# Kernel tuning notes

Measured on AMD Instinct MI355X. Metric: run time of the kernel, lower is better.

## Reference

```python
import jax, jax.numpy as jnp
import numpy as np

NUM_ENTITIES = 40000
NUM_RELATIONS = 500
NUM_EDGES = 400000
ENT_DIM = 50
REL_DIM = 50
NUM_HEADS = 8
UNITS = [150, 300]
NEG_SLOPE = 0.2


def setup_inputs() -> dict:
    key = jax.random.key(0)
    ks = jax.random.split(key, 12)
    h_index = jax.random.randint(ks[0], (NUM_EDGES,), 0, NUM_ENTITIES)
    r_index = jax.random.randint(ks[1], (NUM_EDGES,), 0, NUM_RELATIONS)
    t_index = jax.random.randint(ks[2], (NUM_EDGES,), 0, NUM_ENTITIES)
    std_e = np.sqrt(1.0 / ENT_DIM).astype(np.float32)
    std_r = np.sqrt(1.0 / REL_DIM).astype(np.float32)
    entity_embeddings = jax.random.truncated_normal(ks[3], -2.0, 2.0, (NUM_ENTITIES, ENT_DIM), jnp.float32) * std_e
    relation_embeddings = jax.random.truncated_normal(ks[4], -2.0, 2.0, (NUM_RELATIONS, REL_DIM), jnp.float32) * std_r
    # gat0: input ent dim 50, rel dim 50 -> concat 150, units 150
    c0 = ENT_DIM + REL_DIM + ENT_DIM
    gat0_kernel = jax.random.normal(ks[5], (NUM_HEADS, c0, UNITS[0]), jnp.float32) * (1.0 / np.sqrt(c0))
    gat0_attn = jax.random.normal(ks[6], (NUM_HEADS, UNITS[0]), jnp.float32) * (1.0 / np.sqrt(UNITS[0]))
    gat0_rel_kernel = jax.random.normal(ks[7], (REL_DIM, UNITS[0]), jnp.float32) * (1.0 / np.sqrt(REL_DIM))
    # gat1: input ent dim 8*150=1200, rel dim 150 -> concat 2550, units 300
    e1 = NUM_HEADS * UNITS[0]
    c1 = e1 + UNITS[0] + e1
    gat1_kernel = jax.random.normal(ks[8], (NUM_HEADS, c1, UNITS[1]), jnp.float32) * (1.0 / np.sqrt(c1))
    gat1_attn = jax.random.normal(ks[9], (NUM_HEADS, UNITS[1]), jnp.float32) * (1.0 / np.sqrt(UNITS[1]))
    gat1_rel_kernel = jax.random.normal(ks[10], (UNITS[0], UNITS[1]), jnp.float32) * (1.0 / np.sqrt(UNITS[0]))
    dense_w = jax.random.normal(ks[11], (ENT_DIM, UNITS[1]), jnp.float32) * (1.0 / np.sqrt(ENT_DIM))
    dense_b = jnp.zeros((UNITS[1],), jnp.float32)
    return dict(h_index=h_index, r_index=r_index, t_index=t_index,
                entity_embeddings=entity_embeddings, relation_embeddings=relation_embeddings,
                gat0_kernel=gat0_kernel, gat0_attn=gat0_attn, gat0_rel_kernel=gat0_rel_kernel,
                gat1_kernel=gat1_kernel, gat1_attn=gat1_attn, gat1_rel_kernel=gat1_rel_kernel,
                dense_w=dense_w, dense_b=dense_b)


def _kbgat_layer(h, r, t, ent, rel, kernel, attn, rel_kernel):
    """One KBGAT layer. kernel: [H, De+Dr+De, U] acting on concat(ent[h], rel[r], ent[t]).
    Split kernel so projections happen at node/relation level (equivalent, avoids E x concat_dim)."""
    N = ent.shape[0]
    De = ent.shape[1]
    Dr = rel.shape[1]
    outs = []
    for hd in range(kernel.shape[0]):
        W = kernel[hd]
        Wh, Wr, Wt = W[:De], W[De:De + Dr], W[De + Dr:]
        # message c_{hrt} = W [ent_h ; rel_r ; ent_t] : [E, U]
        c = (ent @ Wh)[h] + (rel @ Wr)[r] + (ent @ Wt)[t]
        s = jax.nn.leaky_relu(c @ attn[hd], NEG_SLOPE)  # [E]
        # segment softmax over triples sharing the same head entity
        m = jax.ops.segment_max(s, h, num_segments=N)
        e = jnp.exp(s - m[h])
        d = jax.ops.segment_sum(e, h, num_segments=N)
        a = e / (d[h] + 1e-10)
        agg = jax.ops.segment_sum(a[:, None] * c, h, num_segments=N)  # [N, U]
        outs.append(jax.nn.elu(agg))
    rel_out = rel @ rel_kernel
    return outs, rel_out


def reference(h_index, r_index, t_index, entity_embeddings, relation_embeddings,
              gat0_kernel, gat0_attn, gat0_rel_kernel,
              gat1_kernel, gat1_attn, gat1_rel_kernel, dense_w, dense_b):
    h = h_index.astype(jnp.int32)
    r = r_index.astype(jnp.int32)
    t = t_index.astype(jnp.int32)
    # dropout rate is 0.0 / inference -> identity
    outs0, rel0 = _kbgat_layer(h, r, t, entity_embeddings, relation_embeddings,
                               gat0_kernel, gat0_attn, gat0_rel_kernel)
    feat = jnp.concatenate(outs0, axis=-1)  # [N, H*U0]
    outs1, rel1 = _kbgat_layer(h, r, t, feat, rel0, gat1_kernel, gat1_attn, gat1_rel_kernel)
    ent_out = outs1[0]
    for o in outs1[1:]:
        ent_out = ent_out + o  # add_n over heads
    ent_out = ent_out + (entity_embeddings @ dense_w + dense_b)  # dense residual
    return ent_out, rel1
```

## Files before the change

kernel.cpp:

```cpp
#include <hip/hip_runtime.h>
#include <hip/hip_bf16.h>
#include <math.h>
#include <stdint.h>

typedef __attribute__((ext_vector_type(8))) __bf16 bf16x8;
typedef __attribute__((ext_vector_type(4))) float f32x4;
typedef unsigned short us;

#define GLP(p) ((__attribute__((address_space(1))) void*)(p))
#define LDP(p) ((__attribute__((address_space(3))) void*)(p))

static __device__ __forceinline__ float b2f(us u) {
    return __uint_as_float(((unsigned int)u) << 16);
}
static __device__ __forceinline__ us f2b(float f) {
    unsigned int x = __float_as_uint(f);
    return (us)((x + 0x7fffu + ((x >> 16) & 1u)) >> 16);
}

__global__ __launch_bounds__(256) void sentinel(float* out, int n, float v) {
    int i = blockIdx.x * 256 + threadIdx.x;
    if (i < n) out[i] = v;
}

__global__ __launch_bounds__(256) void zero_featpad(us* __restrict__ feat) {
    int idx = blockIdx.x * 256 + threadIdx.x;
    if (idx < 40064 * 16) {
        int n = idx >> 4, c = idx & 15;
        feat[(size_t)n * 1216 + 1200 + c] = 0;
    }
}
__global__ __launch_bounds__(256) void zero_x0pad(us* __restrict__ X0) {
    int idx = blockIdx.x * 256 + threadIdx.x;
    if (idx < 4 * 64 * 192) {
        int w = idx / (64 * 192);
        int rem = idx % (64 * 192);
        int rr = rem / 192, c = rem % 192;
        X0[((size_t)w * 40064 + 40000 + rr) * 192 + c] = 0;
    }
}

__global__ __launch_bounds__(256) void count_edges(const int* __restrict__ h, int* __restrict__ counts) {
    int e = blockIdx.x * 256 + threadIdx.x;
    if (e < 400000) atomicAdd(&counts[h[e]], 1);
}

__global__ void scan40k(const int* __restrict__ counts, int* __restrict__ rs) {
    __shared__ int part[1024];
    int tid = threadIdx.x;
    int base = tid * 40;
    int s = 0;
    for (int i = 0; i < 40; ++i) { int idx = base + i; s += (idx < 40000) ? counts[idx] : 0; }
    part[tid] = s;
    __syncthreads();
    for (int off = 1; off < 1024; off <<= 1) {
        int v = (tid >= off) ? part[tid - off] : 0;
        __syncthreads();
        part[tid] += v;
        __syncthreads();
    }
    int run = (tid == 0) ? 0 : part[tid - 1];
    for (int i = 0; i < 40; ++i) {
        int idx = base + i;
        if (idx < 40000) { rs[idx] = run; run += counts[idx]; }
    }
    if (tid == 1023) rs[40000] = part[1023];
}

__global__ __launch_bounds__(256) void scatter_edges(const int* __restrict__ h, const int* __restrict__ rs,
                                                     int* __restrict__ cursor, int* __restrict__ se) {
    int e = blockIdx.x * 256 + threadIdx.x;
    if (e < 400000) {
        int n = h[e];
        int pos = rs[n] + atomicAdd(&cursor[n], 1);
        se[pos] = e;
    }
}

__global__ __launch_bounds__(256) void pack_ent(const float* __restrict__ ent, us* __restrict__ A0) {
    int idx = blockIdx.x * 256 + threadIdx.x;
    if (idx >= 40064 * 64) return;
    int n = idx >> 6, k = idx & 63;
    A0[idx] = (n < 40000 && k < 50) ? f2b(ent[n * 50 + k]) : (us)0;
}

__global__ __launch_bounds__(256) void build_V0(const float* __restrict__ g0k, const float* __restrict__ attn0,
                                                float* __restrict__ V0) {
    int idx = blockIdx.x * 256 + threadIdx.x;
    if (idx >= 50 * 24) return;
    int k = idx / 24, g = idx % 24;
    int part = g >> 3, hd = g & 7;
    int row = k + (part == 1 ? 100 : (part == 2 ? 50 : 0));
    float s = 0.f;
    for (int u = 0; u < 150; ++u)
        s += g0k[(hd * 150 + row) * 150 + u] * attn0[hd * 150 + u];
    V0[idx] = s;
}

__global__ __launch_bounds__(256) void build_VT0(const float* __restrict__ g0k, const float* __restrict__ attn0,
                                                 us* __restrict__ VT0) {
    int idx = blockIdx.x * 256 + threadIdx.x;
    if (idx >= 128 * 64) return;
    int g = idx >> 6, k = idx & 63;
    us v = 0;
    if (g < 16 && k < 50) {
        int part = g >> 3, hd = g & 7;
        int row = part ? (100 + k) : k;
        float s = 0.f;
        for (int u = 0; u < 150; ++u)
            s += g0k[(hd * 150 + row) * 150 + u] * attn0[hd * 150 + u];
        v = f2b(s);
    }
    VT0[idx] = v;
}

__global__ __launch_bounds__(256) void build_VT1(const float* __restrict__ g1k, const float* __restrict__ attn1,
                                                 us* __restrict__ VT1) {
    int idx = blockIdx.x * 256 + threadIdx.x;
    if (idx >= 128 * 1216) return;
    int g = idx / 1216, k = idx % 1216;
    us v = 0;
    if (g < 16 && k < 1200) {
        int part = g >> 3, hd = g & 7;
        int row = part ? (1350 + k) : k;
        float s = 0.f;
        for (int u = 0; u < 300; ++u)
            s += g1k[((size_t)hd * 2550 + row) * 300 + u] * attn1[hd * 300 + u];
        v = f2b(s);
    }
    VT1[idx] = v;
}

__global__ __launch_bounds__(256) void build_Vr1(const float* __restrict__ g1k, const float* __restrict__ attn1,
                                                 float* __restrict__ Vr1) {
    int idx = blockIdx.x * 256 + threadIdx.x;
    if (idx >= 150 * 8) return;
    int k = idx / 8, hd = idx % 8;
    float s = 0.f;
    for (int u = 0; u < 300; ++u)
        s += g1k[((size_t)hd * 2550 + 1200 + k) * 300 + u] * attn1[hd * 300 + u];
    Vr1[idx] = s;
}

__global__ __launch_bounds__(256) void scalar_proj(const void* __restrict__ Av, int aIsF32, int lda, int K,
                                                   const float* __restrict__ V, int ldv, int col0, int G,
                                                   float* __restrict__ out) {
    __shared__ float arow[1216];
    long n = blockIdx.x;
    if (aIsF32) {
        const float* A = (const float*)Av;
        for (int k = threadIdx.x; k < K; k += 256) arow[k] = A[n * lda + k];
    } else {
        const us* A = (const us*)Av;
        for (int k = threadIdx.x; k < K; k += 256) arow[k] = b2f(A[n * lda + k]);
    }
    __syncthreads();
    int g = threadIdx.x >> 4;
    int sl = threadIdx.x & 15;
    if (g < G) {
        float s = 0.f;
        for (int k = sl; k < K; k += 16) s += arow[k] * V[k * ldv + col0 + g];
        for (int off = 8; off; off >>= 1) s += __shfl_down(s, off, 16);
        if (sl == 0) out[n * G + g] = s;
    }
}

__global__ __launch_bounds__(256) void edge_stats(const int* __restrict__ rs, const int* __restrict__ se,
                                                  const int* __restrict__ rIdx, const int* __restrict__ tIdx,
                                                  const float* __restrict__ sc, const float* __restrict__ arr,
                                                  us* __restrict__ eAT, float* __restrict__ sfac) {
    int tid = blockIdx.x * 256 + threadIdx.x;
    if (tid >= 40000 * 8) return;
    int n = tid >> 3, hd = tid & 7;
    float ah = sc[n * 16 + hd];
    int p0 = rs[n], p1 = rs[n + 1];
    float m = -INFINITY, d = 0.f;
    for (int p = p0; p < p1; ++p) {
        int e = se[p];
        float s = ah + arr[rIdx[e] * 8 + hd] + sc[tIdx[e] * 16 + 8 + hd];
        s = (s > 0.f) ? s : 0.2f * s;
        if (s > m) { d = d * expf(m - s) + 1.f; m = s; }
        else d += expf(s - m);
    }
    float inv = 1.f / (d + 1e-10f);
    us* ea = eAT + (size_t)hd * 400000;
    for (int p = p0; p < p1; ++p) {
        int e = se[p];
        float s = ah + arr[rIdx[e] * 8 + hd] + sc[tIdx[e] * 16 + 8 + hd];
        s = (s > 0.f) ? s : 0.2f * s;
        ea[p] = f2b(expf(s - m) * inv);
    }
    sfac[tid] = d * inv;
}

__global__ __launch_bounds__(256) void agg0x4(int g, const int* __restrict__ rs, const int* __restrict__ se,
                                              const int* __restrict__ rIdx, const int* __restrict__ tIdx,
                                              const us* __restrict__ eAT, const float* __restrict__ sfac,
                                              const float* __restrict__ ent, const float* __restrict__ rel,
                                              us* __restrict__ X0) {
    __shared__ int sr[128], st[128];
    __shared__ float sa[4][128];
    long n = blockIdx.x;
    int tid = threadIdx.x;
    int lane = tid & 63, wave = tid >> 6;
    int hd = 4 * g + wave;
    int k = lane;
    float ev = (k < 50) ? ent[n * 50 + k] : 0.f;
    float xh = sfac[n * 8 + hd] * ev;
    float ra = 0.f, ta = 0.f;
    int p0 = rs[n], p1 = rs[n + 1];
    for (int c0 = p0; c0 < p1; c0 += 128) {
        int cnt = min(128, p1 - c0);
        __syncthreads();
        if (tid < cnt) {
            int e = se[c0 + tid];
            sr[tid] = rIdx[e];
            st[tid] = tIdx[e];
#pragma unroll
            for (int w = 0; w < 4; ++w)
                sa[w][tid] = b2f(eAT[(size_t)(4 * g + w) * 400000 + c0 + tid]);
        }
        __syncthreads();
#pragma unroll 2
        for (int i = 0; i < cnt; ++i) {
            float a = sa[wave][i];
            int r = sr[i], t = st[i];
            if (k < 50) {
                ra += a * rel[r * 50 + k];
                ta += a * ent[(long)t * 50 + k];
            }
        }
    }
    us* row = X0 + ((size_t)wave * 40064 + n) * 192;
    if (k < 50) { row[k] = f2b(xh); row[50 + k] = f2b(ra); row[100 + k] = f2b(ta); }
    if (lane < 42) row[150 + lane] = 0;
}

__global__ __launch_bounds__(256) void build_B0T8(const float* __restrict__ g0k, us* __restrict__ B) {
    int idx = blockIdx.x * 256 + threadIdx.x;
    if (idx >= 8 * 256 * 192) return;
    int hd = idx / (256 * 192);
    int u = (idx / 192) % 256, k = idx % 192;
    us v = 0;
    if (u < 150 && k < 150) v = f2b(g0k[((size_t)hd * 150 + k) * 150 + u]);
    B[idx] = v;
}

__global__ __launch_bounds__(256) void build_B1Th2(int g, const float* __restrict__ g1k, us* __restrict__ B) {
    int idx = blockIdx.x * 256 + threadIdx.x;
    if (idx >= 1280 * 1216) return;
    int j = idx / 1216, k = idx % 1216;
    us v = 0;
    if (j < 1216 && k < 1200) {
        int blk = j / 304, u = j % 304;
        if (u < 300) {
            int hd = 2 * g + (blk & 1);
            int row = (blk >= 2) ? (1350 + k) : k;
            v = f2b(g1k[((size_t)hd * 2550 + row) * 300 + u]);
        }
    }
    B[idx] = v;
}

#define GEMM_BODY(EPILOG)                                                                       \
    __shared__ __align__(16) us As[2][128 * 64];                                                \
    __shared__ __align__(16) us Bs[2][128 * 64];                                                \
    const int tid = threadIdx.x;                                                                \
    const int lane = tid & 63, wave = tid >> 6;                                                 \
    const int wr = wave >> 1, wc = wave & 1;                                                    \
    const int r16 = lane & 15, g4 = lane >> 4;                                                  \
    const long bm = blockIdx.y, bn = blockIdx.x;                                                \
    f32x4 acc[4][4];                                                                            \
    _Pragma("unroll") for (int m = 0; m < 4; ++m)                                               \
        _Pragma("unroll") for (int n = 0; n < 4; ++n) acc[m][n] = (f32x4){0.f, 0.f, 0.f, 0.f};  \
    auto stage = [&](int buf, int kt) {                                                         \
        _Pragma("unroll") for (int i = 0; i < 4; ++i) {                                         \
            int idx = tid + i * 256;                                                            \
            int row = idx >> 3, sub = idx & 7;                                                  \
            int scol = ((sub ^ (row & 7)) << 3);                                                \
            const us* ga = A + (bm * 128 + row) * (long)K + kt + scol;                          \
            __builtin_amdgcn_global_load_lds(GLP(ga), LDP(&As[buf][idx * 8]), 16, 0, 0);        \
        }                                                                                       \
        _Pragma("unroll") for (int i = 0; i < 4; ++i) {                                         \
            int idx = tid + i * 256;                                                            \
            int row = idx >> 3, sub = idx & 7;                                                  \
            int scol = ((sub ^ (row & 7)) << 3);                                                \
            const us* gb = BT + (bn * 128 + row) * (long)K + kt + scol;                         \
            __builtin_amdgcn_global_load_lds(GLP(gb), LDP(&Bs[buf][idx * 8]), 16, 0, 0);        \
        }                                                                                       \
    };                                                                                          \
    const int nt = K >> 6;                                                                      \
    stage(0, 0);                                                                                \
    const int sxor = (r16 & 7) << 3;                                                            \
    for (int t = 0; t < nt; ++t) {                                                              \
        int cur = t & 1;                                                                        \
        if (t + 1 < nt) {                                                                       \
            stage(cur ^ 1, (t + 1) << 6);                                                       \
            asm volatile("s_waitcnt vmcnt(8)" ::: "memory");                                    \
        } else {                                                                                \
            asm volatile("s_waitcnt vmcnt(0)" ::: "memory");                                    \
        }                                                                                       \
        __builtin_amdgcn_s_barrier();                                                           \
        asm volatile("" ::: "memory");                                                          \
        _Pragma("unroll") for (int kk = 0; kk < 2; ++kk) {                                      \
            bf16x8 af[4], bfr[4];                                                               \
            _Pragma("unroll") for (int m = 0; m < 4; ++m)                                       \
                af[m] = *(const bf16x8*)&As[cur][(wr * 64 + m * 16 + r16) * 64 +                \
                                               ((kk * 32 + g4 * 8) ^ sxor)];                    \
            _Pragma("unroll") for (int n = 0; n < 4; ++n)                                       \
                bfr[n] = *(const bf16x8*)&Bs[cur][(wc * 64 + n * 16 + r16) * 64 +               \
                                                ((kk * 32 + g4 * 8) ^ sxor)];                   \
            _Pragma("unroll") for (int m = 0; m < 4; ++m)                                       \
                _Pragma("unroll") for (int n = 0; n < 4; ++n)                                   \
                    acc[m][n] = __builtin_amdgcn_mfma_f32_16x16x32_bf16(af[m], bfr[n],          \
                                                                        acc[m][n], 0, 0, 0);    \
        }                                                                                       \
        asm volatile("" ::: "memory");                                                          \
        __builtin_amdgcn_s_barrier();                                                           \
    }                                                                                           \
    _Pragma("unroll") for (int m = 0; m < 4; ++m)                                               \
        _Pragma("unroll") for (int n = 0; n < 4; ++n)                                           \
            _Pragma("unroll") for (int j = 0; j < 4; ++j) { EPILOG }

__global__ __launch_bounds__(256) void gemm_bt(const us* __restrict__ A_, const us* __restrict__ BT_,
                                               us* __restrict__ C, int K, int ldc, int nColReal,
                                               int colOff0, int colOffZ, long aStrideZ, long btStrideZ,
                                               int act) {
    const int z = blockIdx.z;
    const us* A = A_ + (size_t)z * aStrideZ;
    const us* BT = BT_ + (size_t)z * btStrideZ;
    const int colBase = colOff0 + z * colOffZ;
    GEMM_BODY(
        int cc = (int)bn * 128 + wc * 64 + n * 16 + r16;
        if (cc < nColReal) {
            long row = bm * 128 + wr * 64 + m * 16 + g4 * 4 + j;
            float v = acc[m][n][j];
            if (act) v = (v > 0.f) ? v : expm1f(v);
            C[row * (long)ldc + colBase + cc] = f2b(v);
        })
}

__global__ __launch_bounds__(256) void gemm_bt_f32(const us* __restrict__ A, const us* __restrict__ BT,
                                                   float* __restrict__ C, int K, int ldc, int nColReal) {
    GEMM_BODY(
        int cc = (int)bn * 128 + wc * 64 + n * 16 + r16;
        if (cc < nColReal) {
            long row = bm * 128 + wr * 64 + m * 16 + g4 * 4 + j;
            C[row * (long)ldc + cc] = acc[m][n][j];
        })
}

__global__ __launch_bounds__(256) void rel0_kernel(const float* __restrict__ rel, const float* __restrict__ g0rk,
                                                   float* __restrict__ rel0b) {
    int idx = blockIdx.x * 256 + threadIdx.x;
    if (idx >= 500 * 150) return;
    int rI = idx / 150, u = idx % 150;
    float s = 0.f;
    for (int k = 0; k < 50; ++k) s += rel[rI * 50 + k] * g0rk[k * 150 + u];
    rel0b[idx] = s;
}

__global__ __launch_bounds__(256) void pr1_kernel(const float* __restrict__ rel0b, const float* __restrict__ g1k,
                                                  float* __restrict__ PR1) {
    int idx = blockIdx.x * 256 + threadIdx.x;
    if (idx >= 500 * 2400) return;
    int rI = idx / 2400, jj = idx % 2400;
    int hd = jj / 300, u = jj % 300;
    float s = 0.f;
    for (int k = 0; k < 150; ++k)
        s += rel0b[rI * 150 + k] * g1k[((size_t)hd * 2550 + 1200 + k) * 300 + u];
    PR1[idx] = s;
}

__global__ __launch_bounds__(256) void rel1_kernel(const float* __restrict__ rel0b, const float* __restrict__ g1rk,
                                                   float* __restrict__ out) {
    int idx = blockIdx.x * 256 + threadIdx.x;
    if (idx >= 500 * 300) return;
    int rI = idx / 300, u = idx % 300;
    float s = 0.f;
    for (int k = 0; k < 150; ++k) s += rel0b[rI * 150 + k] * g1rk[k * 300 + u];
    out[idx] = s;
}

__global__ __launch_bounds__(256) void out_init(const float* __restrict__ ent, const float* __restrict__ dw,
                                                const float* __restrict__ db, float* __restrict__ outAcc) {
    int idx = blockIdx.x * 256 + threadIdx.x;
    if (idx >= 40000 * 300) return;
    int n = idx / 300, u = idx % 300;
    float s = db[u];
    for (int k = 0; k < 50; ++k) s += ent[n * 50 + k] * dw[k * 300 + u];
    outAcc[idx] = s;
}

__global__ __launch_bounds__(256) void agg1h2(int g, const int* __restrict__ rs, const int* __restrict__ se,
                                              const int* __restrict__ rIdx, const int* __restrict__ tIdx,
                                              const us* __restrict__ eAT, const float* __restrict__ sfac,
                                              const us* __restrict__ C1g2, const float* __restrict__ PR1,
                                              float* __restrict__ outf) {
    __shared__ int sr[128], st[128];
    __shared__ float sa0[128], sa1[128];
    long n = blockIdx.x;
    int tid = threadIdx.x;
    int hd0 = 2 * g, hd1 = hd0 + 1;
    int d = tid, d2 = tid + 256;
    bool a2 = (d2 < 300);
    float sf0 = sfac[n * 8 + hd0], sf1 = sfac[n * 8 + hd1];
    const us* crow = C1g2 + (size_t)n * 1216;
    float acc00 = sf0 * b2f(crow[d]);
    float acc10 = sf1 * b2f(crow[304 + d]);
    float acc01 = a2 ? sf0 * b2f(crow[d2]) : 0.f;
    float acc11 = a2 ? sf1 * b2f(crow[304 + d2]) : 0.f;
    const us* ea0 = eAT + (size_t)hd0 * 400000;
    const us* ea1 = eAT + (size_t)hd1 * 400000;
    int p0 = rs[n], p1 = rs[n + 1];
    for (int c0 = p0; c0 < p1; c0 += 128) {
        int cnt = min(128, p1 - c0);
        __syncthreads();
        if (tid < cnt) {
            int e = se[c0 + tid];
            sr[tid] = rIdx[e];
            st[tid] = tIdx[e];
            sa0[tid] = b2f(ea0[c0 + tid]);
            sa1[tid] = b2f(ea1[c0 + tid]);
        }
        __syncthreads();
#pragma unroll 2
        for (int i = 0; i < cnt; ++i) {
            int r = sr[i], t = st[i];
            float a0 = sa0[i], a1 = sa1[i];
            const us* ct = C1g2 + (size_t)t * 1216;
            const float* pr = PR1 + (size_t)r * 2400;
            acc00 += a0 * (pr[hd0 * 300 + d] + b2f(ct[608 + d]));
            acc10 += a1 * (pr[hd1 * 300 + d] + b2f(ct[912 + d]));
            if (a2) {
                acc01 += a0 * (pr[hd0 * 300 + d2] + b2f(ct[608 + d2]));
                acc11 += a1 * (pr[hd1 * 300 + d2] + b2f(ct[912 + d2]));
            }
        }
    }
    float v00 = (acc00 > 0.f) ? acc00 : expm1f(acc00);
    float v10 = (acc10 > 0.f) ? acc10 : expm1f(acc10);
    outf[n * 300 + d] += v00 + v10;
    if (a2) {
        float v01 = (acc01 > 0.f) ? acc01 : expm1f(acc01);
        float v11 = (acc11 > 0.f) ? acc11 : expm1f(acc11);
        outf[n * 300 + d2] += v01 + v11;
    }
}

extern "C" void kernel_launch(void* const* d_in, const int* in_sizes, int n_in,
                              void* d_out, int out_size, void* d_ws, size_t ws_size,
                              hipStream_t stream) {
    const int* hIdx = (const int*)d_in[0];
    const int* rIdx = (const int*)d_in[1];
    const int* tIdx = (const int*)d_in[2];
    const float* ent  = (const float*)d_in[3];
    const float* rel  = (const float*)d_in[4];
    const float* g0k  = (const float*)d_in[5];
    const float* at0w = (const float*)d_in[6];
    const float* g0rk = (const float*)d_in[7];
    const float* g1k  = (const float*)d_in[8];
    const float* at1w = (const float*)d_in[9];
    const float* g1rk = (const float*)d_in[10];
    const float* dw   = (const float*)d_in[11];
    const float* db   = (const float*)d_in[12];
    float* outf = (float*)d_out;

    {
        const int exp_sz[13] = {400000, 400000, 400000, 2000000, 25000, 180000, 1200,
                                7500, 6120000, 2400, 45000, 15000, 300};
        bool ok = (n_in == 13);
        for (int i = 0; ok && i < 13; ++i) ok = (in_sizes[i] == exp_sz[i]);
        if (!ok) {
            sentinel<<<(out_size + 255) / 256, 256, 0, stream>>>(outf, out_size, 44.0f);
            return;
        }
    }

    char* p = (char*)d_ws;
    auto carve = [&](size_t bytes) -> char* {
        char* r = p;
        p += (bytes + 255) & ~(size_t)255;
        return r;
    };
    int* counts = (int*)carve(40000 * 4);
    int* cursor = (int*)carve(40000 * 4);
    int* rs     = (int*)carve(40001 * 4);
    int* se     = (int*)carve(400000 * 4);
    float* sc   = (float*)carve((size_t)40064 * 16 * 4);
    float* arS  = (float*)carve(500 * 8 * 4);
    us* eAT     = (us*)carve((size_t)8 * 400000 * 2);
    float* sfac = (float*)carve((size_t)40000 * 8 * 4);
    float* V0  = (float*)carve(50 * 24 * 4);
    float* Vr1 = (float*)carve(150 * 8 * 4);
    float* rel0b = (float*)carve(500 * 150 * 4);
    float* PR1 = (float*)carve((size_t)500 * 2400 * 4);
    us* VT0   = (us*)carve((size_t)128 * 64 * 2);
    us* VT1   = (us*)carve((size_t)128 * 1216 * 2);
    us* B0T8  = (us*)carve((size_t)8 * 256 * 192 * 2);
    us* B1Th2 = (us*)carve((size_t)1280 * 1216 * 2);
    us* feat  = (us*)carve((size_t)40064 * 1216 * 2);
    char* tail = p;
    us* A0   = (us*)tail;
    us* X0   = (us*)tail;
    us* C1g2 = (us*)tail;
    size_t tailNeed = (size_t)40064 * 1216 * 2;
    size_t totalNeed = (size_t)(tail - (char*)d_ws) + tailNeed;
    if (totalNeed > ws_size) {
        sentinel<<<(out_size + 255) / 256, 256, 0, stream>>>(outf, out_size, 42.0f);
        return;
    }

    hipMemsetAsync(counts, 0, 40000 * 4, stream);
    hipMemsetAsync(cursor, 0, 40000 * 4, stream);
    zero_featpad<<<(40064 * 16 + 255) / 256, 256, 0, stream>>>(feat);

    count_edges<<<1563, 256, 0, stream>>>(hIdx, counts);
    scan40k<<<1, 1024, 0, stream>>>(counts, rs);
    scatter_edges<<<1563, 256, 0, stream>>>(hIdx, rs, cursor, se);

    pack_ent<<<(40064 * 64 + 255) / 256, 256, 0, stream>>>(ent, A0);
    build_VT0<<<(128 * 64 + 255) / 256, 256, 0, stream>>>(g0k, at0w, VT0);
    gemm_bt_f32<<<dim3(1, 313), 256, 0, stream>>>(A0, VT0, sc, 64, 16, 16);
    build_V0<<<5, 256, 0, stream>>>(g0k, at0w, V0);
    scalar_proj<<<500, 256, 0, stream>>>(rel, 1, 50, 50, V0, 24, 16, 8, arS);
    edge_stats<<<1250, 256, 0, stream>>>(rs, se, rIdx, tIdx, sc, arS, eAT, sfac);

    zero_x0pad<<<(4 * 64 * 192 + 255) / 256, 256, 0, stream>>>(X0);
    build_B0T8<<<(8 * 256 * 192 + 255) / 256, 256, 0, stream>>>(g0k, B0T8);
    for (int g = 0; g < 2; ++g) {
        agg0x4<<<40000, 256, 0, stream>>>(g, rs, se, rIdx, tIdx, eAT, sfac, ent, rel, X0);
        gemm_bt<<<dim3(2, 313, 4), 256, 0, stream>>>(X0, B0T8 + (size_t)g * 4 * 256 * 192, feat,
                                                     192, 1216, 150, g * 600, 150,
                                                     (long)40064 * 192, (long)256 * 192, 1);
    }

    rel0_kernel<<<(500 * 150 + 255) / 256, 256, 0, stream>>>(rel, g0rk, rel0b);
    build_VT1<<<(128 * 1216 + 255) / 256, 256, 0, stream>>>(g1k, at1w, VT1);
    build_Vr1<<<5, 256, 0, stream>>>(g1k, at1w, Vr1);
    gemm_bt_f32<<<dim3(1, 313), 256, 0, stream>>>(feat, VT1, sc, 1216, 16, 16);
    scalar_proj<<<500, 256, 0, stream>>>(rel0b, 1, 150, 150, Vr1, 8, 0, 8, arS);
    edge_stats<<<1250, 256, 0, stream>>>(rs, se, rIdx, tIdx, sc, arS, eAT, sfac);
    pr1_kernel<<<(500 * 2400 + 255) / 256, 256, 0, stream>>>(rel0b, g1k, PR1);

    out_init<<<(40000 * 300 + 255) / 256, 256, 0, stream>>>(ent, dw, db, outf);

    for (int g = 0; g < 4; ++g) {
        build_B1Th2<<<(1280 * 1216 + 255) / 256, 256, 0, stream>>>(g, g1k, B1Th2);
        gemm_bt<<<dim3(10, 313, 1), 256, 0, stream>>>(feat, B1Th2, C1g2,
                                                      1216, 1216, 1216, 0, 0, 0, 0, 0);
        agg1h2<<<40000, 256, 0, stream>>>(g, rs, se, rIdx, tIdx, eAT, sfac, C1g2, PR1, outf);
    }

    rel1_kernel<<<(500 * 300 + 255) / 256, 256, 0, stream>>>(rel0b, g1rk, outf + (size_t)40000 * 300);
}
```

Measured before the change: 2.191 ms.

## Remap GEMM tiles across XCDs, use MFMA for residual, store PR1 in bf16

The GEMM macro now remaps workgroup IDs so consecutive tiles land on the same XCD, improving L2 reuse. It also raises wave priority around the MFMA loop. The scalar out_init residual kernel is replaced by an MFMA GEMM on the packed entity matrix against a transposed bf16 dense weight, with a bias epilogue. PR1 is stored in bf16 to halve gather traffic in agg1h2, and the unroll factors in the two aggregation loops are raised. These changes lower precision on the residual and PR1 paths and rely on rel1 overwriting the padded rows the residual GEMM writes.

```diff
diff --git a/kernel.cpp b/kernel.cpp
--- a/kernel.cpp
+++ b/kernel.cpp
@@ -140,6 +140,15 @@
     for (int u = 0; u < 300; ++u)
         s += g1k[((size_t)hd * 2550 + 1200 + k) * 300 + u] * attn1[hd * 300 + u];
     Vr1[idx] = s;
+}
+
+__global__ __launch_bounds__(256) void build_dwT(const float* __restrict__ dw, us* __restrict__ dwT) {
+    int idx = blockIdx.x * 256 + threadIdx.x;
+    if (idx >= 384 * 64) return;
+    int j = idx >> 6, k = idx & 63;
+    us v = 0;
+    if (j < 300 && k < 50) v = f2b(dw[k * 300 + j]);
+    dwT[idx] = v;
 }
 
 __global__ __launch_bounds__(256) void scalar_proj(const void* __restrict__ Av, int aIsF32, int lda, int K,
@@ -221,7 +230,7 @@
                 sa[w][tid] = b2f(eAT[(size_t)(4 * g + w) * 400000 + c0 + tid]);
         }
         __syncthreads();
-#pragma unroll 2
+#pragma unroll 4
         for (int i = 0; i < cnt; ++i) {
             float a = sa[wave][i];
             int r = sr[i], t = st[i];
@@ -269,7 +278,13 @@
     const int lane = tid & 63, wave = tid >> 6;                                                 \
     const int wr = wave >> 1, wc = wave & 1;                                                    \
     const int r16 = lane & 15, g4 = lane >> 4;                                                  \
-    const long bm = blockIdx.y, bn = blockIdx.x;                                                \
+    const int gx = gridDim.x;                                                                   \
+    const int nwg = gx * gridDim.y;                                                             \
+    const int orig = blockIdx.y * gx + blockIdx.x;                                              \
+    const int q8 = nwg >> 3, r8 = nwg & 7;                                                      \
+    const int xcd = orig & 7;                                                                   \
+    const int lg = (xcd < r8 ? xcd * (q8 + 1) : r8 * (q8 + 1) + (xcd - r8) * q8) + (orig >> 3); \
+    const long bm = lg / gx, bn = lg % gx;                                                      \
     f32x4 acc[4][4];                                                                            \
     _Pragma("unroll") for (int m = 0; m < 4; ++m)                                               \
         _Pragma("unroll") for (int n = 0; n < 4; ++n) acc[m][n] = (f32x4){0.f, 0.f, 0.f, 0.f};  \
@@ -302,6 +317,7 @@
         }                                                                                       \
         __builtin_amdgcn_s_barrier();                                                           \
         asm volatile("" ::: "memory");                                                          \
+        __builtin_amdgcn_s_setprio(1);                                                          \
         _Pragma("unroll") for (int kk = 0; kk < 2; ++kk) {                                      \
             bf16x8 af[4], bfr[4];                                                               \
             _Pragma("unroll") for (int m = 0; m < 4; ++m)                                       \
@@ -315,6 +331,7 @@
                     acc[m][n] = __builtin_amdgcn_mfma_f32_16x16x32_bf16(af[m], bfr[n],          \
                                                                         acc[m][n], 0, 0, 0);    \
         }                                                                                       \
+        __builtin_amdgcn_s_setprio(0);                                                          \
         asm volatile("" ::: "memory");                                                          \
         __builtin_amdgcn_s_barrier();                                                           \
     }                                                                                           \
@@ -341,12 +358,15 @@
 }
 
 __global__ __launch_bounds__(256) void gemm_bt_f32(const us* __restrict__ A, const us* __restrict__ BT,
-                                                   float* __restrict__ C, int K, int ldc, int nColReal) {
+                                                   float* __restrict__ C, int K, int ldc, int nColReal,
+                                                   const float* __restrict__ bias) {
     GEMM_BODY(
         int cc = (int)bn * 128 + wc * 64 + n * 16 + r16;
         if (cc < nColReal) {
             long row = bm * 128 + wr * 64 + m * 16 + g4 * 4 + j;
-            C[row * (long)ldc + cc] = acc[m][n][j];
+            float v = acc[m][n][j];
+            if (bias) v += bias[cc];
+            C[row * (long)ldc + cc] = v;
         })
 }
 
@@ -361,7 +381,7 @@
 }
 
 __global__ __launch_bounds__(256) void pr1_kernel(const float* __restrict__ rel0b, const float* __restrict__ g1k,
-                                                  float* __restrict__ PR1) {
+                                                  us* __restrict__ PR1b) {
     int idx = blockIdx.x * 256 + threadIdx.x;
     if (idx >= 500 * 2400) return;
     int rI = idx / 2400, jj = idx % 2400;
@@ -369,7 +389,7 @@
     float s = 0.f;
     for (int k = 0; k < 150; ++k)
         s += rel0b[rI * 150 + k] * g1k[((size_t)hd * 2550 + 1200 + k) * 300 + u];
-    PR1[idx] = s;
+    PR1b[idx] = f2b(s);
 }
 
 __global__ __launch_bounds__(256) void rel1_kernel(const float* __restrict__ rel0b, const float* __restrict__ g1rk,
@@ -382,20 +402,10 @@
     out[idx] = s;
 }
 
-__global__ __launch_bounds__(256) void out_init(const float* __restrict__ ent, const float* __restrict__ dw,
-                                                const float* __restrict__ db, float* __restrict__ outAcc) {
-    int idx = blockIdx.x * 256 + threadIdx.x;
-    if (idx >= 40000 * 300) return;
-    int n = idx / 300, u = idx % 300;
-    float s = db[u];
-    for (int k = 0; k < 50; ++k) s += ent[n * 50 + k] * dw[k * 300 + u];
-    outAcc[idx] = s;
-}
-
 __global__ __launch_bounds__(256) void agg1h2(int g, const int* __restrict__ rs, const int* __restrict__ se,
                                               const int* __restrict__ rIdx, const int* __restrict__ tIdx,
                                               const us* __restrict__ eAT, const float* __restrict__ sfac,
-                                              const us* __restrict__ C1g2, const float* __restrict__ PR1,
+                                              const us* __restrict__ C1g2, const us* __restrict__ PR1b,
                                               float* __restrict__ outf) {
     __shared__ int sr[128], st[128];
     __shared__ float sa0[128], sa1[128];
@@ -424,17 +434,17 @@
             sa1[tid] = b2f(ea1[c0 + tid]);
         }
         __syncthreads();
-#pragma unroll 2
+#pragma unroll 4
         for (int i = 0; i < cnt; ++i) {
             int r = sr[i], t = st[i];
             float a0 = sa0[i], a1 = sa1[i];
             const us* ct = C1g2 + (size_t)t * 1216;
-            const float* pr = PR1 + (size_t)r * 2400;
-            acc00 += a0 * (pr[hd0 * 300 + d] + b2f(ct[608 + d]));
-            acc10 += a1 * (pr[hd1 * 300 + d] + b2f(ct[912 + d]));
+            const us* pr = PR1b + (size_t)r * 2400;
+            acc00 += a0 * (b2f(pr[hd0 * 300 + d]) + b2f(ct[608 + d]));
+            acc10 += a1 * (b2f(pr[hd1 * 300 + d]) + b2f(ct[912 + d]));
             if (a2) {
-                acc01 += a0 * (pr[hd0 * 300 + d2] + b2f(ct[608 + d2]));
-                acc11 += a1 * (pr[hd1 * 300 + d2] + b2f(ct[912 + d2]));
+                acc01 += a0 * (b2f(pr[hd0 * 300 + d2]) + b2f(ct[608 + d2]));
+                acc11 += a1 * (b2f(pr[hd1 * 300 + d2]) + b2f(ct[912 + d2]));
             }
         }
     }
@@ -494,9 +504,10 @@
     float* V0  = (float*)carve(50 * 24 * 4);
     float* Vr1 = (float*)carve(150 * 8 * 4);
     float* rel0b = (float*)carve(500 * 150 * 4);
-    float* PR1 = (float*)carve((size_t)500 * 2400 * 4);
+    us* PR1b  = (us*)carve((size_t)500 * 2400 * 2);
     us* VT0   = (us*)carve((size_t)128 * 64 * 2);
     us* VT1   = (us*)carve((size_t)128 * 1216 * 2);
+    us* dwT   = (us*)carve((size_t)384 * 64 * 2);
     us* B0T8  = (us*)carve((size_t)8 * 256 * 192 * 2);
     us* B1Th2 = (us*)carve((size_t)1280 * 1216 * 2);
     us* feat  = (us*)carve((size_t)40064 * 1216 * 2);
@@ -521,7 +532,9 @@
 
     pack_ent<<<(40064 * 64 + 255) / 256, 256, 0, stream>>>(ent, A0);
     build_VT0<<<(128 * 64 + 255) / 256, 256, 0, stream>>>(g0k, at0w, VT0);
-    gemm_bt_f32<<<dim3(1, 313), 256, 0, stream>>>(A0, VT0, sc, 64, 16, 16);
+    gemm_bt_f32<<<dim3(1, 313), 256, 0, stream>>>(A0, VT0, sc, 64, 16, 16, nullptr);
+    build_dwT<<<(384 * 64 + 255) / 256, 256, 0, stream>>>(dw, dwT);
+    gemm_bt_f32<<<dim3(3, 313), 256, 0, stream>>>(A0, dwT, outf, 64, 300, 300, db);
     build_V0<<<5, 256, 0, stream>>>(g0k, at0w, V0);
     scalar_proj<<<500, 256, 0, stream>>>(rel, 1, 50, 50, V0, 24, 16, 8, arS);
     edge_stats<<<1250, 256, 0, stream>>>(rs, se, rIdx, tIdx, sc, arS, eAT, sfac);
@@ -538,18 +551,16 @@
     rel0_kernel<<<(500 * 150 + 255) / 256, 256, 0, stream>>>(rel, g0rk, rel0b);
     build_VT1<<<(128 * 1216 + 255) / 256, 256, 0, stream>>>(g1k, at1w, VT1);
     build_Vr1<<<5, 256, 0, stream>>>(g1k, at1w, Vr1);
-    gemm_bt_f32<<<dim3(1, 313), 256, 0, stream>>>(feat, VT1, sc, 1216, 16, 16);
+    gemm_bt_f32<<<dim3(1, 313), 256, 0, stream>>>(feat, VT1, sc, 1216, 16, 16, nullptr);
     scalar_proj<<<500, 256, 0, stream>>>(rel0b, 1, 150, 150, Vr1, 8, 0, 8, arS);
     edge_stats<<<1250, 256, 0, stream>>>(rs, se, rIdx, tIdx, sc, arS, eAT, sfac);
-    pr1_kernel<<<(500 * 2400 + 255) / 256, 256, 0, stream>>>(rel0b, g1k, PR1);
-
-    out_init<<<(40000 * 300 + 255) / 256, 256, 0, stream>>>(ent, dw, db, outf);
+    pr1_kernel<<<(500 * 2400 + 255) / 256, 256, 0, stream>>>(rel0b, g1k, PR1b);
 
     for (int g = 0; g < 4; ++g) {
         build_B1Th2<<<(1280 * 1216 + 255) / 256, 256, 0, stream>>>(g, g1k, B1Th2);
         gemm_bt<<<dim3(10, 313, 1), 256, 0, stream>>>(feat, B1Th2, C1g2,
                                                       1216, 1216, 1216, 0, 0, 0, 0, 0);
-        agg1h2<<<40000, 256, 0, stream>>>(g, rs, se, rIdx, tIdx, eAT, sfac, C1g2, PR1, outf);
+        agg1h2<<<40000, 256, 0, stream>>>(g, rs, se, rIdx, tIdx, eAT, sfac, C1g2, PR1b, outf);
     }
 
     rel1_kernel<<<(500 * 300 + 255) / 256, 256, 0, stream>>>(rel0b, g1rk, outf + (size_t)40000 * 300);
```

Result: faster. 1.968 ms (-10.1%).
